# Performance work log

Hardware: AMD Instinct MI355X
Metric: run time of the kernel (lower is better)

## Reference

```python
import jax, jax.numpy as jnp
import numpy as np

N_NODES = 100000
N_EDGES = 1600000
D_FEAT = 256
HID = 128
DEG_DIM = 128  # data.degree_exist_matrix.shape[1]


def setup_inputs() -> dict:
    key = jax.random.key(0)
    ks = jax.random.split(key, 12)
    s = lambda fan_in: 1.0 / np.sqrt(fan_in)
    x = jax.random.normal(ks[0], (N_NODES, D_FEAT), dtype=jnp.float32)
    edge_index = jax.random.randint(ks[1], (2, N_EDGES), 0, N_NODES, dtype=jnp.int32)
    return {
        "x": x,
        "edge_index": edge_index,
        # GCNConv 1 / 2 (PyG stores weight [in,out], bias [out])
        "W1": jax.random.uniform(ks[2], (D_FEAT, HID), jnp.float32, -s(D_FEAT), s(D_FEAT)),
        "b1": jnp.zeros((HID,), jnp.float32),
        "W2": jax.random.uniform(ks[3], (HID, HID), jnp.float32, -s(HID), s(HID)),
        "b2": jnp.zeros((HID,), jnp.float32),
        # down_sample Linear(D_FEAT, HID)
        "Wd": jax.random.uniform(ks[4], (D_FEAT, HID), jnp.float32, -s(D_FEAT), s(D_FEAT)),
        "bd": jax.random.uniform(ks[5], (HID,), jnp.float32, -s(D_FEAT), s(D_FEAT)),
        # linear2: Degree_layer(HID, 1) ~ Linear(HID, 1)
        "Wdeg": jax.random.uniform(ks[6], (HID, 1), jnp.float32, -s(HID), s(HID)),
        "bdeg": jax.random.uniform(ks[7], (1,), jnp.float32, -s(HID), s(HID)),
        # linear3: Linear(HID, DEG_DIM)
        "W3": jax.random.uniform(ks[8], (HID, DEG_DIM), jnp.float32, -s(HID), s(HID)),
        "b3": jax.random.uniform(ks[9], (DEG_DIM,), jnp.float32, -s(HID), s(HID)),
    }


def gcn_conv(x, W, b, src, dst, n):
    """PyG GCNConv: D^-1/2 (A+I) D^-1/2 X W + b (symmetric norm, self-loops)."""
    h = x @ W  # [N, out]
    deg = jax.ops.segment_sum(jnp.ones_like(dst, dtype=h.dtype), dst, num_segments=n) + 1.0
    dinv = jax.lax.rsqrt(deg)  # deg >= 1 from self loop
    coef = dinv[src] * dinv[dst]  # [E]
    msgs = h[src] * coef[:, None]  # [E, out] -- dominant gather
    agg = jax.ops.segment_sum(msgs, dst, num_segments=n)
    agg = agg + h * (dinv * dinv)[:, None]  # self-loop contribution
    return agg + b


def reference(x, edge_index, W1, b1, W2, b2, Wd, bd, Wdeg, bdeg, W3, b3):
    n = x.shape[0]
    src, dst = edge_index[0], edge_index[1]
    original_x = x @ Wd + bd
    h = gcn_conv(x, W1, b1, src, dst, n)
    h = jax.nn.relu(h)  # dropout is identity in eval mode
    h = gcn_conv(h, W2, b2, src, dst, n)
    h = h + original_x  # residual
    result1 = jax.nn.log_softmax(h, axis=-1)        # [N, HID]
    result2 = (h @ Wdeg + bdeg).squeeze(-1)          # [N]
    result3 = h @ W3 + b3                            # [N, DEG_DIM]
    return (result1, result2, result3)
```

## Files before the change

kernel.cpp:

```cpp
#include <hip/hip_runtime.h>


typedef __attribute__((ext_vector_type(8))) short bf16x8;
typedef __attribute__((ext_vector_type(4))) float f32x4;

#define CDIV(a, b) (((a) + (b) - 1) / (b))

#define GLOBAL_AS __attribute__((address_space(1)))
#define LDS_AS __attribute__((address_space(3)))

__device__ __forceinline__ void gload16(const void* g, void* l) {
  __builtin_amdgcn_global_load_lds((const GLOBAL_AS unsigned int*)g,
                                   (LDS_AS unsigned int*)l, 16, 0, 0);
}

__device__ __forceinline__ float b2f(unsigned short u) {
  union { unsigned int i; float f; } x; x.i = ((unsigned int)u) << 16; return x.f;
}
__device__ __forceinline__ unsigned short f2b(float f) {
  union { float f; unsigned int i; } x; x.f = f;
  unsigned int r = x.i + 0x7fffu + ((x.i >> 16) & 1u);
  return (unsigned short)(r >> 16);
}
__device__ __forceinline__ void add2(float& a0, float& a1, unsigned int u) {
  union { unsigned int i; float f; } lo, hi;
  lo.i = u << 16; hi.i = u & 0xffff0000u;
  a0 += lo.f; a1 += hi.f;
}
__device__ __forceinline__ unsigned int pack2(float lo, float hi) {
  return __builtin_amdgcn_perm(__float_as_uint(hi) + 0x8000u,
                               __float_as_uint(lo) + 0x8000u, 0x07060302u);
}


__global__ void k_wtrans4(const float* __restrict__ W1, const float* __restrict__ Wd,
                          const float* __restrict__ W2, const float* __restrict__ W3,
                          unsigned short* __restrict__ W1t, unsigned short* __restrict__ Wdt,
                          unsigned short* __restrict__ W2t, unsigned short* __restrict__ W3t,
                          int* __restrict__ deg, int* __restrict__ bcnt, int n) {
  int idx = blockIdx.x * blockDim.x + threadIdx.x;
  if (idx >= 98304) {
    idx -= 98304;
    if (idx < n) deg[idx] = 0;
    else if (idx - n < 512) bcnt[idx - n] = 0;
    return;
  }
  const float* in; unsigned short* out; int K, N;
  if (idx < 32768)       { in = W1; out = W1t; K = 256; N = 128; }
  else if (idx < 65536)  { in = Wd; out = Wdt; K = 256; N = 128; idx -= 32768; }
  else if (idx < 81920)  { in = W2; out = W2t; K = 128; N = 128; idx -= 65536; }
  else                   { in = W3; out = W3t; K = 128; N = 128; idx -= 81920; }
  int k = idx / N, nn = idx - k * N;
  out[nn * K + k] = f2b(in[idx]);
}

__global__ void k_scan1(const int* __restrict__ deg, int* __restrict__ lscan,
                        int* __restrict__ partials, float* __restrict__ dinv, int n) {
  __shared__ int sd[256];
  int tid = threadIdx.x;
  int base = blockIdx.x * 2048 + tid * 8;
  int v[8]; int tsum = 0;
#pragma unroll
  for (int i = 0; i < 8; ++i) {
    int idx = base + i;
    int xv = (idx < n) ? deg[idx] : 0;
    v[i] = xv; tsum += xv;
    if (idx < n) dinv[idx] = 1.0f / sqrtf((float)xv + 1.0f);
  }
  sd[tid] = tsum;
  __syncthreads();
  for (int off = 1; off < 256; off <<= 1) {
    int t = (tid >= off) ? sd[tid - off] : 0;
    __syncthreads();
    sd[tid] += t;
    __syncthreads();
  }
  int run = sd[tid] - tsum;
#pragma unroll
  for (int i = 0; i < 8; ++i) {
    int idx = base + i;
    if (idx < n) lscan[idx] = run;
    run += v[i];
  }
  if (tid == 255) partials[blockIdx.x] = sd[255];
}

__global__ void k_scan3(const int* __restrict__ partials, int* row_start,
                        int* __restrict__ cursor, int n, int E) {
  int idx = blockIdx.x * blockDim.x + threadIdx.x;
  if (idx >= n) return;
  int g = idx >> 11;
  int pre = 0;
  for (int i = 0; i < g; ++i) pre += partials[i];
  int v = row_start[idx] + pre;
  row_start[idx] = v;
  cursor[idx] = v;
  if (idx == 0) row_start[n] = E;
}


#define BIN_CHUNK 4096
#define OVF_CAP 65536

__global__ __launch_bounds__(256) void k_binA(
    const int* __restrict__ ei, int E, int nbuck, int cap,
    int* __restrict__ deg, int2* __restrict__ pairs, int* __restrict__ bcnt,
    int2* __restrict__ ovf, int* __restrict__ ovf_cnt) {
  __shared__ int lcnt[256];
  __shared__ int lbase[256];
  int tid = threadIdx.x;
  for (int i = tid; i < nbuck; i += 256) lcnt[i] = 0;
  __syncthreads();
  int base_e = blockIdx.x * BIN_CHUNK;
  int src[16], dst[16], lofs[16];
#pragma unroll
  for (int i = 0; i < 16; ++i) {
    int e = base_e + i * 256 + tid;
    if (e < E) {
      int s = ei[e], d = ei[E + e];
      src[i] = s; dst[i] = d;
      atomicAdd(&deg[d], 1);
      lofs[i] = atomicAdd(&lcnt[d >> 9], 1);
    } else {
      dst[i] = -1;
    }
  }
  __syncthreads();
  for (int b = tid; b < nbuck; b += 256)
    lbase[b] = atomicAdd(&bcnt[b], lcnt[b]);
  __syncthreads();
#pragma unroll
  for (int i = 0; i < 16; ++i) {
    if (dst[i] < 0) continue;
    int b = dst[i] >> 9;
    int gpos = lbase[b] + lofs[i];
    if (gpos < cap) {
      pairs[(size_t)b * cap + gpos] = make_int2(src[i], dst[i]);
    } else {
      int op = atomicAdd(ovf_cnt, 1);
      if (op < OVF_CAP) ovf[op] = make_int2(src[i], dst[i]);
    }
  }
}

__global__ __launch_bounds__(256) void k_binB(
    const int2* __restrict__ pairs, const int* __restrict__ bcnt,
    int nbuck, int cap,
    const int2* __restrict__ ovf, const int* __restrict__ ovf_cnt,
    int* __restrict__ cursor, int* __restrict__ csr_src, int n) {
  int ov = *ovf_cnt;
  if ((int)blockIdx.x < nbuck) {
    int b = blockIdx.x;
    int cnt = bcnt[b]; if (cnt > cap) cnt = cap;
    const int2* p = pairs + (size_t)b * cap;
    if (ov == 0) {
      __shared__ int lcur[512];
      int nbase = b << 9;
      for (int i = threadIdx.x; i < 512; i += 256) {
        int node = nbase + i;
        lcur[i] = (node < n) ? cursor[node] : 0;
      }
      __syncthreads();
      for (int i = threadIdx.x; i < cnt; i += 256) {
        int2 e = p[i];
        int pos = atomicAdd(&lcur[e.y - nbase], 1);
        csr_src[pos] = e.x;
      }
    } else {
      for (int i = threadIdx.x; i < cnt; i += 256) {
        int2 e = p[i];
        int pos = atomicAdd(&cursor[e.y], 1);
        csr_src[pos] = e.x;
      }
    }
  } else {
    int total = ov; if (total > OVF_CAP) total = OVF_CAP;
    int start = (blockIdx.x - nbuck) * 256 + threadIdx.x;
    for (int i = start; i < total; i += 8 * 256) {
      int2 e = ovf[i];
      int pos = atomicAdd(&cursor[e.y], 1);
      csr_src[pos] = e.x;
    }
  }
}


__global__ __launch_bounds__(512) void k_gemm_x2(
    const float* __restrict__ X,
    const unsigned short* __restrict__ B1t,
    const unsigned short* __restrict__ B2t,
    const float* __restrict__ bias2,
    const float* __restrict__ dinvp,
    unsigned short* __restrict__ O1,
    unsigned short* __restrict__ O2,
    int n) {
  __shared__ char lds[65536];
  const int flat = threadIdx.x;
  const int wave = flat >> 6, lane = flat & 63;
  const int l15 = lane & 15, q = lane >> 4;
  const int wM = wave >> 1, wN = wave & 1;
  const int rowBase = blockIdx.x * 128;
  const int colBase = wN * 64;

  auto stage = [&](int kb, int buf) {
    char* ldsA = lds + buf * 32768;
    char* ldsB = ldsA + 16384;
    const char* Xb = (const char*)X;
#pragma unroll
    for (int j = 0; j < 2; ++j) {
      int i = j * 512 + flat;
      int row = i >> 3, pslot = i & 7;
      int lslot = pslot ^ (row & 7);
      int rowc = rowBase + row; if (rowc >= n) rowc = n - 1;
      gload16(Xb + (size_t)rowc * 1024 + (size_t)(kb * 128 + lslot * 16),
              ldsA + (j * 512 + wave * 64) * 16);
    }
#pragma unroll
    for (int j = 0; j < 2; ++j) {
      int i = j * 512 + flat;
      int col = i >> 3, pslot = i & 7;
      int lslot = pslot ^ (col & 7);
      const char* src = (lslot >= 4) ? (const char*)B2t : (const char*)B1t;
      gload16(src + (size_t)col * 512 + kb * 64 + (lslot & 3) * 16,
              ldsB + (j * 512 + wave * 64) * 16);
    }
  };

  f32x4 acc1[2][4], acc2[2][4];
#pragma unroll
  for (int i = 0; i < 2; ++i)
#pragma unroll
    for (int j = 0; j < 4; ++j) {
      acc1[i][j] = (f32x4){0.f, 0.f, 0.f, 0.f};
      acc2[i][j] = (f32x4){0.f, 0.f, 0.f, 0.f};
    }

  stage(0, 0);
  stage(1, 1);

#pragma unroll
  for (int kb = 0; kb < 8; ++kb) {
    int cur = kb & 1;
    if (kb < 7) asm volatile("s_waitcnt vmcnt(4)" ::: "memory");
    else        asm volatile("s_waitcnt vmcnt(0)" ::: "memory");
    __builtin_amdgcn_s_barrier();
    char* ldsA = lds + cur * 32768;
    char* ldsB = ldsA + 16384;
    bf16x8 a[2], b1v[4], b2v[4];
#pragma unroll
    for (int mt = 0; mt < 2; ++mt) {
      int row = wM * 32 + mt * 16 + l15;
      uint4 lo = *(const uint4*)(ldsA + row * 128 + (((2 * q) ^ (row & 7)) * 16));
      uint4 hi = *(const uint4*)(ldsA + row * 128 + (((2 * q + 1) ^ (row & 7)) * 16));
      union { bf16x8 v; unsigned int u[4]; } r;
      r.u[0] = __builtin_amdgcn_perm(lo.y + 0x8000u, lo.x + 0x8000u, 0x07060302u);
      r.u[1] = __builtin_amdgcn_perm(lo.w + 0x8000u, lo.z + 0x8000u, 0x07060302u);
      r.u[2] = __builtin_amdgcn_perm(hi.y + 0x8000u, hi.x + 0x8000u, 0x07060302u);
      r.u[3] = __builtin_amdgcn_perm(hi.w + 0x8000u, hi.z + 0x8000u, 0x07060302u);
      a[mt] = r.v;
    }
#pragma unroll
    for (int nt = 0; nt < 4; ++nt) {
      int col = colBase + nt * 16 + l15;
      b1v[nt] = *(const bf16x8*)(ldsB + col * 128 + ((q ^ (col & 7)) * 16));
      b2v[nt] = *(const bf16x8*)(ldsB + col * 128 + (((4 + q) ^ (col & 7)) * 16));
    }
#pragma unroll
    for (int mt = 0; mt < 2; ++mt)
#pragma unroll
      for (int nt = 0; nt < 4; ++nt) {
        acc1[mt][nt] = __builtin_amdgcn_mfma_f32_16x16x32_bf16(a[mt], b1v[nt], acc1[mt][nt], 0, 0, 0);
        acc2[mt][nt] = __builtin_amdgcn_mfma_f32_16x16x32_bf16(a[mt], b2v[nt], acc2[mt][nt], 0, 0, 0);
      }
    asm volatile("s_waitcnt lgkmcnt(0)" ::: "memory");
    __builtin_amdgcn_s_barrier();
    if (kb < 6) stage(kb + 2, cur);
  }

#pragma unroll
  for (int mt = 0; mt < 2; ++mt) {
    float4 dv = *(const float4*)(dinvp + rowBase + wM * 32 + mt * 16 + q * 4);
#pragma unroll
    for (int nt = 0; nt < 4; ++nt) {
      int col = colBase + nt * 16 + l15;
      float bb = bias2[col];
#pragma unroll
      for (int r = 0; r < 4; ++r) {
        int row = rowBase + wM * 32 + mt * 16 + q * 4 + r;
        if (row < n) {
          float dvr = (r == 0) ? dv.x : (r == 1) ? dv.y : (r == 2) ? dv.z : dv.w;
          O1[(size_t)row * 128 + col] = f2b(acc1[mt][nt][r] * dvr);
          O2[(size_t)row * 128 + col] = f2b(acc2[mt][nt][r] + bb);
        }
      }
    }
  }
}

template <int OUT_F32>
__global__ __launch_bounds__(512) void k_gemm_h(
    const unsigned short* __restrict__ X, const unsigned short* __restrict__ Bt,
    const float* __restrict__ bias, const float* __restrict__ dinvp,
    unsigned short* __restrict__ Ob, float* __restrict__ Of, int n) {
  __shared__ char lds[65536];
  const int flat = threadIdx.x;
  const int wave = flat >> 6, lane = flat & 63;
  const int l15 = lane & 15, q = lane >> 4;
  const int wM = wave >> 1, wN = wave & 1;
  const int rowBase = blockIdx.x * 128;
  const int colBase = wN * 64;

  auto stage = [&](int ks, int buf) {
    char* ldsA = lds + buf * 32768;
    char* ldsB = ldsA + 16384;
#pragma unroll
    for (int j = 0; j < 2; ++j) {
      int i = j * 512 + flat;
      int row = i >> 3, pslot = i & 7;
      int lslot = pslot ^ (row & 7);
      int rowc = rowBase + row; if (rowc >= n) rowc = n - 1;
      gload16((const char*)X + (size_t)rowc * 256 + ks * 128 + lslot * 16,
              ldsA + (j * 512 + wave * 64) * 16);
    }
#pragma unroll
    for (int j = 0; j < 2; ++j) {
      int i = j * 512 + flat;
      int col = i >> 3, pslot = i & 7;
      int lslot = pslot ^ (col & 7);
      gload16((const char*)Bt + (size_t)col * 256 + ks * 128 + lslot * 16,
              ldsB + (j * 512 + wave * 64) * 16);
    }
  };

  f32x4 acc[2][4];
#pragma unroll
  for (int i = 0; i < 2; ++i)
#pragma unroll
    for (int j = 0; j < 4; ++j) acc[i][j] = (f32x4){0.f, 0.f, 0.f, 0.f};

  stage(0, 0);
  stage(1, 1);

#pragma unroll
  for (int ks = 0; ks < 2; ++ks) {
    if (ks == 0) asm volatile("s_waitcnt vmcnt(4)" ::: "memory");
    else         asm volatile("s_waitcnt vmcnt(0)" ::: "memory");
    __builtin_amdgcn_s_barrier();
    char* ldsA = lds + ks * 32768;
    char* ldsB = ldsA + 16384;
#pragma unroll
    for (int k2 = 0; k2 < 2; ++k2) {
      bf16x8 a[2], b[4];
#pragma unroll
      for (int mt = 0; mt < 2; ++mt) {
        int row = wM * 32 + mt * 16 + l15;
        a[mt] = *(const bf16x8*)(ldsA + row * 128 + (((k2 * 4 + q) ^ (row & 7)) * 16));
      }
#pragma unroll
      for (int nt = 0; nt < 4; ++nt) {
        int col = colBase + nt * 16 + l15;
        b[nt] = *(const bf16x8*)(ldsB + col * 128 + (((k2 * 4 + q) ^ (col & 7)) * 16));
      }
#pragma unroll
      for (int mt = 0; mt < 2; ++mt)
#pragma unroll
        for (int nt = 0; nt < 4; ++nt)
          acc[mt][nt] = __builtin_amdgcn_mfma_f32_16x16x32_bf16(a[mt], b[nt], acc[mt][nt], 0, 0, 0);
    }
  }

#pragma unroll
  for (int mt = 0; mt < 2; ++mt) {
    float4 dv;
    if (!OUT_F32) dv = *(const float4*)(dinvp + rowBase + wM * 32 + mt * 16 + q * 4);
#pragma unroll
    for (int nt = 0; nt < 4; ++nt) {
      int col = colBase + nt * 16 + l15;
      float bb = OUT_F32 ? bias[col] : 0.f;
#pragma unroll
      for (int r = 0; r < 4; ++r) {
        int row = rowBase + wM * 32 + mt * 16 + q * 4 + r;
        if (row < n) {
          if (OUT_F32) {
            __builtin_nontemporal_store(acc[mt][nt][r] + bb, &Of[(size_t)row * 128 + col]);
          } else {
            float dvr = (r == 0) ? dv.x : (r == 1) ? dv.y : (r == 2) ? dv.z : dv.w;
            Ob[(size_t)row * 128 + col] = f2b(acc[mt][nt][r] * dvr);
          }
        }
      }
    }
  }
}


__device__ __forceinline__ void agg_edges4(
    const unsigned short* __restrict__ h, const int* __restrict__ csr_src,
    int beg, int end, int lane, int grp, int sub, float* acc) {
  for (int base = beg; base < end; base += 64) {
    int m = end - base; if (m > 64) m = 64;
    int idx_l = (base + lane < end) ? csr_src[base + lane] : 0;
    for (int j = 0; j < m; j += 16) {
      int s0 = __builtin_amdgcn_ds_bpermute((j + grp) << 2, idx_l);
      int s1 = __builtin_amdgcn_ds_bpermute((j + 4 + grp) << 2, idx_l);
      int s2 = __builtin_amdgcn_ds_bpermute((j + 8 + grp) << 2, idx_l);
      int s3 = __builtin_amdgcn_ds_bpermute((j + 12 + grp) << 2, idx_l);
      uint4 v0 = *(const uint4*)(h + (size_t)s0 * 128 + sub * 8);
      uint4 v1 = *(const uint4*)(h + (size_t)s1 * 128 + sub * 8);
      uint4 v2 = *(const uint4*)(h + (size_t)s2 * 128 + sub * 8);
      uint4 v3 = *(const uint4*)(h + (size_t)s3 * 128 + sub * 8);
      if (j + grp < m) {
        add2(acc[0], acc[1], v0.x); add2(acc[2], acc[3], v0.y);
        add2(acc[4], acc[5], v0.z); add2(acc[6], acc[7], v0.w);
      }
      if (j + 4 + grp < m) {
        add2(acc[0], acc[1], v1.x); add2(acc[2], acc[3], v1.y);
        add2(acc[4], acc[5], v1.z); add2(acc[6], acc[7], v1.w);
      }
      if (j + 8 + grp < m) {
        add2(acc[0], acc[1], v2.x); add2(acc[2], acc[3], v2.y);
        add2(acc[4], acc[5], v2.z); add2(acc[6], acc[7], v2.w);
      }
      if (j + 12 + grp < m) {
        add2(acc[0], acc[1], v3.x); add2(acc[2], acc[3], v3.y);
        add2(acc[4], acc[5], v3.z); add2(acc[6], acc[7], v3.w);
      }
    }
  }
}

__device__ __forceinline__ void grp_reduce(float* acc) {
#pragma unroll
  for (int i = 0; i < 8; ++i) {
    acc[i] += __shfl_xor(acc[i], 16);
    acc[i] += __shfl_xor(acc[i], 32);
  }
}

__global__ __launch_bounds__(256) void k_agg1(
    const unsigned short* __restrict__ h,
    const int* __restrict__ row_start, const int* __restrict__ csr_src,
    const float* __restrict__ dinv,
    const float* __restrict__ bias,
    unsigned short* __restrict__ hout, int n) {
  int gw = blockIdx.x * 4 + (threadIdx.x >> 6);
  int lane = threadIdx.x & 63;
  int grp = lane >> 4, sub = lane & 15;
  if (gw >= n) return;
  int beg = row_start[gw], end = row_start[gw + 1];
  float acc[8] = {0.f, 0.f, 0.f, 0.f, 0.f, 0.f, 0.f, 0.f};
  agg_edges4(h, csr_src, beg, end, lane, grp, sub, acc);
  grp_reduce(acc);
  if (grp == 0) {
    float dg = dinv[gw];
    uint4 sv = *(const uint4*)(h + (size_t)gw * 128 + sub * 8);
    add2(acc[0], acc[1], sv.x); add2(acc[2], acc[3], sv.y);
    add2(acc[4], acc[5], sv.z); add2(acc[6], acc[7], sv.w);
    float4 b0 = *(const float4*)(bias + sub * 8);
    float4 b1v = *(const float4*)(bias + sub * 8 + 4);
    float a[8];
    a[0] = fmaxf(acc[0] * dg + b0.x, 0.f); a[1] = fmaxf(acc[1] * dg + b0.y, 0.f);
    a[2] = fmaxf(acc[2] * dg + b0.z, 0.f); a[3] = fmaxf(acc[3] * dg + b0.w, 0.f);
    a[4] = fmaxf(acc[4] * dg + b1v.x, 0.f); a[5] = fmaxf(acc[5] * dg + b1v.y, 0.f);
    a[6] = fmaxf(acc[6] * dg + b1v.z, 0.f); a[7] = fmaxf(acc[7] * dg + b1v.w, 0.f);
    uint4 o;
    o.x = pack2(a[0], a[1]); o.y = pack2(a[2], a[3]);
    o.z = pack2(a[4], a[5]); o.w = pack2(a[6], a[7]);
    *(uint4*)(hout + (size_t)gw * 128 + sub * 8) = o;
  }
}

__global__ __launch_bounds__(256) void k_agg2_epi(
    const unsigned short* __restrict__ h,
    const int* __restrict__ row_start, const int* __restrict__ csr_src,
    const float* __restrict__ dinv,
    const float* __restrict__ bias,
    const unsigned short* __restrict__ resb,
    float* __restrict__ out1,
    const float* __restrict__ wdeg, const float* __restrict__ bdeg,
    float* __restrict__ out2,
    unsigned short* __restrict__ hf,
    int n) {
  int gw = blockIdx.x * 4 + (threadIdx.x >> 6);
  int lane = threadIdx.x & 63;
  int grp = lane >> 4, sub = lane & 15;
  if (gw >= n) return;
  int beg = row_start[gw], end = row_start[gw + 1];
  float acc[8] = {0.f, 0.f, 0.f, 0.f, 0.f, 0.f, 0.f, 0.f};
  agg_edges4(h, csr_src, beg, end, lane, grp, sub, acc);
  grp_reduce(acc);
  if (grp == 0) {
    float dg = dinv[gw];
    uint4 sv = *(const uint4*)(h + (size_t)gw * 128 + sub * 8);
    add2(acc[0], acc[1], sv.x); add2(acc[2], acc[3], sv.y);
    add2(acc[4], acc[5], sv.z); add2(acc[6], acc[7], sv.w);
    float4 b0 = *(const float4*)(bias + sub * 8);
    float4 b1v = *(const float4*)(bias + sub * 8 + 4);
    uint4 rv = *(const uint4*)(resb + (size_t)gw * 128 + sub * 8);
    float a[8];
    a[0] = acc[0] * dg + b0.x; a[1] = acc[1] * dg + b0.y;
    a[2] = acc[2] * dg + b0.z; a[3] = acc[3] * dg + b0.w;
    a[4] = acc[4] * dg + b1v.x; a[5] = acc[5] * dg + b1v.y;
    a[6] = acc[6] * dg + b1v.z; a[7] = acc[7] * dg + b1v.w;
    add2(a[0], a[1], rv.x); add2(a[2], a[3], rv.y);
    add2(a[4], a[5], rv.z); add2(a[6], a[7], rv.w);
    uint4 o;
    o.x = pack2(a[0], a[1]); o.y = pack2(a[2], a[3]);
    o.z = pack2(a[4], a[5]); o.w = pack2(a[6], a[7]);
    *(uint4*)(hf + (size_t)gw * 128 + sub * 8) = o;
    float4 w0 = *(const float4*)(wdeg + sub * 8);
    float4 w1 = *(const float4*)(wdeg + sub * 8 + 4);
    float t = a[0] * w0.x + a[1] * w0.y + a[2] * w0.z + a[3] * w0.w +
              a[4] * w1.x + a[5] * w1.y + a[6] * w1.z + a[7] * w1.w;
#pragma unroll
    for (int mk = 8; mk >= 1; mk >>= 1) t += __shfl_xor(t, mk);
    if (sub == 0) __builtin_nontemporal_store(t + bdeg[0], out2 + gw);
    float mx = a[0];
#pragma unroll
    for (int i = 1; i < 8; ++i) mx = fmaxf(mx, a[i]);
#pragma unroll
    for (int mk = 8; mk >= 1; mk >>= 1) mx = fmaxf(mx, __shfl_xor(mx, mk));
    float l = 0.f;
#pragma unroll
    for (int i = 0; i < 8; ++i) l += __expf(a[i] - mx);
#pragma unroll
    for (int mk = 8; mk >= 1; mk >>= 1) l += __shfl_xor(l, mk);
    float ls = mx + __logf(l);
    f32x4 o0 = {a[0] - ls, a[1] - ls, a[2] - ls, a[3] - ls};
    f32x4 o1 = {a[4] - ls, a[5] - ls, a[6] - ls, a[7] - ls};
    __builtin_nontemporal_store(o0, (f32x4*)(out1 + (size_t)gw * 128 + sub * 8));
    __builtin_nontemporal_store(o1, (f32x4*)(out1 + (size_t)gw * 128 + sub * 8 + 4));
  }
}


extern "C" void kernel_launch(void* const* d_in, const int* in_sizes, int n_in,
                              void* d_out, int out_size, void* d_ws, size_t ws_size,
                              hipStream_t stream) {
  const float* x   = (const float*)d_in[0];
  const int*   ei  = (const int*)d_in[1];
  const float* W1  = (const float*)d_in[2];
  const float* b1  = (const float*)d_in[3];
  const float* W2  = (const float*)d_in[4];
  const float* b2  = (const float*)d_in[5];
  const float* Wd  = (const float*)d_in[6];
  const float* bd  = (const float*)d_in[7];
  const float* Wdg = (const float*)d_in[8];
  const float* bdg = (const float*)d_in[9];
  const float* W3  = (const float*)d_in[10];
  const float* b3  = (const float*)d_in[11];

  const int N = in_sizes[0] / 256;
  const int E = in_sizes[1] / 2;

  char* w = (char*)d_ws;
  auto alloc = [&](size_t bytes) {
    char* p = w;
    w += (bytes + 255) & ~(size_t)255;
    return p;
  };
  unsigned short* W1t  = (unsigned short*)alloc((size_t)256 * 128 * 2);
  unsigned short* Wdt  = (unsigned short*)alloc((size_t)256 * 128 * 2);
  unsigned short* W2t  = (unsigned short*)alloc((size_t)128 * 128 * 2);
  unsigned short* W3t  = (unsigned short*)alloc((size_t)128 * 128 * 2);
  unsigned short* bufC = (unsigned short*)alloc((size_t)N * 128 * 2);
  int*   deg      = (int*)alloc((size_t)N * 4);
  float* dinv     = (float*)alloc((size_t)(N + 128) * 4);
  int*   row_start= (int*)alloc((size_t)(N + 1) * 4);
  int*   cursor   = (int*)alloc((size_t)N * 4);
  int*   partials = (int*)alloc(4096);
  int*   csr_src  = (int*)alloc((size_t)E * 4);
  int*   bcnt     = (int*)alloc(2048);
  int*   ovf_cnt  = bcnt + 256;
  int2*  ovf      = (int2*)alloc((size_t)OVF_CAP * 8);

  float* out1 = (float*)d_out;
  float* out2 = out1 + (size_t)N * 128;
  float* out3 = out2 + (size_t)N;
  unsigned short* bufA = (unsigned short*)out3;
  unsigned short* resb = bufA + (size_t)N * 128;

  const int nbuck = CDIV(N, 512);
  int cap = (E / nbuck) + (E / nbuck) / 2;
  cap = (cap + 255) & ~255;
  size_t bufC_bytes = (size_t)N * 128 * 2;
  if ((size_t)nbuck * cap * 8 > bufC_bytes)
    cap = (int)(bufC_bytes / ((size_t)nbuck * 8));
  int2* pairs = (int2*)bufC;

  k_wtrans4<<<CDIV(98304 + N + 512, 256), 256, 0, stream>>>(
      W1, Wd, W2, W3, W1t, Wdt, W2t, W3t, deg, bcnt, N);

  k_binA<<<CDIV(E, BIN_CHUNK), 256, 0, stream>>>(ei, E, nbuck, cap, deg, pairs,
                                                 bcnt, ovf, ovf_cnt);

  const int nb = CDIV(N, 2048);
  k_scan1<<<nb, 256, 0, stream>>>(deg, row_start, partials, dinv, N);
  k_scan3<<<CDIV(N, 256), 256, 0, stream>>>(partials, row_start, cursor, N, E);

  k_gemm_x2<<<CDIV(N, 128), 512, 0, stream>>>(x, W1t, Wdt, bd, dinv, bufA, resb, N);

  k_binB<<<nbuck + 8, 256, 0, stream>>>(pairs, bcnt, nbuck, cap, ovf, ovf_cnt,
                                        cursor, csr_src, N);

  k_agg1<<<CDIV(N, 4), 256, 0, stream>>>(bufA, row_start, csr_src, dinv, b1, bufC, N);

  k_gemm_h<0><<<CDIV(N, 128), 512, 0, stream>>>(bufC, W2t, nullptr, dinv, bufA, nullptr, N);

  k_agg2_epi<<<CDIV(N, 4), 256, 0, stream>>>(bufA, row_start, csr_src, dinv,
                                             b2, resb, out1, Wdg, bdg, out2, bufC, N);

  k_gemm_h<1><<<CDIV(N, 128), 512, 0, stream>>>(bufC, W3t, b3, nullptr, nullptr, out3, N);
}
```

Baseline: 497.3 us.

## Fuse degree count, scan and CSR scatter into one per-bucket kernel

```diff
diff --git a/kernel.cpp b/kernel.cpp
--- a/kernel.cpp
+++ b/kernel.cpp
@@ -37,12 +37,11 @@
                           const float* __restrict__ W2, const float* __restrict__ W3,
                           unsigned short* __restrict__ W1t, unsigned short* __restrict__ Wdt,
                           unsigned short* __restrict__ W2t, unsigned short* __restrict__ W3t,
-                          int* __restrict__ deg, int* __restrict__ bcnt, int n) {
+                          int* __restrict__ bcnt) {
   int idx = blockIdx.x * blockDim.x + threadIdx.x;
   if (idx >= 98304) {
     idx -= 98304;
-    if (idx < n) deg[idx] = 0;
-    else if (idx - n < 512) bcnt[idx - n] = 0;
+    if (idx < 512) bcnt[idx] = 0;
     return;
   }
   const float* in; unsigned short* out; int K, N;
@@ -54,57 +53,13 @@
   out[nn * K + k] = f2b(in[idx]);
 }
 
-__global__ void k_scan1(const int* __restrict__ deg, int* __restrict__ lscan,
-                        int* __restrict__ partials, float* __restrict__ dinv, int n) {
-  __shared__ int sd[256];
-  int tid = threadIdx.x;
-  int base = blockIdx.x * 2048 + tid * 8;
-  int v[8]; int tsum = 0;
-#pragma unroll
-  for (int i = 0; i < 8; ++i) {
-    int idx = base + i;
-    int xv = (idx < n) ? deg[idx] : 0;
-    v[i] = xv; tsum += xv;
-    if (idx < n) dinv[idx] = 1.0f / sqrtf((float)xv + 1.0f);
-  }
-  sd[tid] = tsum;
-  __syncthreads();
-  for (int off = 1; off < 256; off <<= 1) {
-    int t = (tid >= off) ? sd[tid - off] : 0;
-    __syncthreads();
-    sd[tid] += t;
-    __syncthreads();
-  }
-  int run = sd[tid] - tsum;
-#pragma unroll
-  for (int i = 0; i < 8; ++i) {
-    int idx = base + i;
-    if (idx < n) lscan[idx] = run;
-    run += v[i];
-  }
-  if (tid == 255) partials[blockIdx.x] = sd[255];
-}
-
-__global__ void k_scan3(const int* __restrict__ partials, int* row_start,
-                        int* __restrict__ cursor, int n, int E) {
-  int idx = blockIdx.x * blockDim.x + threadIdx.x;
-  if (idx >= n) return;
-  int g = idx >> 11;
-  int pre = 0;
-  for (int i = 0; i < g; ++i) pre += partials[i];
-  int v = row_start[idx] + pre;
-  row_start[idx] = v;
-  cursor[idx] = v;
-  if (idx == 0) row_start[n] = E;
-}
-
 
 #define BIN_CHUNK 4096
 #define OVF_CAP 65536
 
 __global__ __launch_bounds__(256) void k_binA(
     const int* __restrict__ ei, int E, int nbuck, int cap,
-    int* __restrict__ deg, int2* __restrict__ pairs, int* __restrict__ bcnt,
+    int2* __restrict__ pairs, int* __restrict__ bcnt,
     int2* __restrict__ ovf, int* __restrict__ ovf_cnt) {
   __shared__ int lcnt[256];
   __shared__ int lbase[256];
@@ -119,7 +74,6 @@
     if (e < E) {
       int s = ei[e], d = ei[E + e];
       src[i] = s; dst[i] = d;
-      atomicAdd(&deg[d], 1);
       lofs[i] = atomicAdd(&lcnt[d >> 9], 1);
     } else {
       dst[i] = -1;
@@ -143,43 +97,78 @@
   }
 }
 
-__global__ __launch_bounds__(256) void k_binB(
+__global__ __launch_bounds__(256) void k_binBC(
     const int2* __restrict__ pairs, const int* __restrict__ bcnt,
     int nbuck, int cap,
     const int2* __restrict__ ovf, const int* __restrict__ ovf_cnt,
-    int* __restrict__ cursor, int* __restrict__ csr_src, int n) {
-  int ov = *ovf_cnt;
-  if ((int)blockIdx.x < nbuck) {
-    int b = blockIdx.x;
-    int cnt = bcnt[b]; if (cnt > cap) cnt = cap;
-    const int2* p = pairs + (size_t)b * cap;
-    if (ov == 0) {
-      __shared__ int lcur[512];
-      int nbase = b << 9;
-      for (int i = threadIdx.x; i < 512; i += 256) {
-        int node = nbase + i;
-        lcur[i] = (node < n) ? cursor[node] : 0;
-      }
-      __syncthreads();
-      for (int i = threadIdx.x; i < cnt; i += 256) {
-        int2 e = p[i];
-        int pos = atomicAdd(&lcur[e.y - nbase], 1);
+    float* __restrict__ dinv, int* __restrict__ row_start,
+    int* __restrict__ csr_src, int n, int E) {
+  __shared__ int hist[512];
+  __shared__ int sb[256];
+  const int b = blockIdx.x;
+  const int tid = threadIdx.x;
+  const int nbase = b << 9;
+  hist[tid] = 0; hist[tid + 256] = 0;
+  __syncthreads();
+  int total = bcnt[b];
+  int cnt = (total < cap) ? total : cap;
+  const int2* p = pairs + (size_t)b * cap;
+  for (int i = tid; i < cnt; i += 256)
+    atomicAdd(&hist[p[i].y - nbase], 1);
+  int ov = *ovf_cnt; if (ov > OVF_CAP) ov = OVF_CAP;
+  if (ov > 0) {
+    for (int i = tid; i < ov; i += 256) {
+      int2 e = ovf[i];
+      if ((e.y >> 9) == b) atomicAdd(&hist[e.y - nbase], 1);
+    }
+  }
+  __syncthreads();
+  int h0 = hist[2 * tid], h1 = hist[2 * tid + 1];
+  sb[tid] = (tid < nbuck) ? bcnt[tid] : 0;
+  __syncthreads();
+  for (int off = 1; off < 256; off <<= 1) {
+    int t = (tid >= off) ? sb[tid - off] : 0;
+    __syncthreads();
+    sb[tid] += t;
+    __syncthreads();
+  }
+  int gbase = (b > 0) ? sb[b - 1] : 0;
+  __syncthreads();
+  sb[tid] = h0 + h1;
+  __syncthreads();
+  for (int off = 1; off < 256; off <<= 1) {
+    int t = (tid >= off) ? sb[tid - off] : 0;
+    __syncthreads();
+    sb[tid] += t;
+    __syncthreads();
+  }
+  int exc = (tid > 0) ? sb[tid - 1] : 0;
+  int c0 = gbase + exc, c1 = gbase + exc + h0;
+  int node0 = nbase + 2 * tid, node1 = node0 + 1;
+  if (node0 < n) {
+    dinv[node0] = 1.0f / sqrtf((float)h0 + 1.0f);
+    row_start[node0] = c0;
+  }
+  if (node1 < n) {
+    dinv[node1] = 1.0f / sqrtf((float)h1 + 1.0f);
+    row_start[node1] = c1;
+  }
+  if (b == 0 && tid == 0) row_start[n] = E;
+  __syncthreads();
+  hist[2 * tid] = c0; hist[2 * tid + 1] = c1;
+  __syncthreads();
+  for (int i = tid; i < cnt; i += 256) {
+    int2 e = p[i];
+    int pos = atomicAdd(&hist[e.y - nbase], 1);
+    csr_src[pos] = e.x;
+  }
+  if (ov > 0) {
+    for (int i = tid; i < ov; i += 256) {
+      int2 e = ovf[i];
+      if ((e.y >> 9) == b) {
+        int pos = atomicAdd(&hist[e.y - nbase], 1);
         csr_src[pos] = e.x;
       }
-    } else {
-      for (int i = threadIdx.x; i < cnt; i += 256) {
-        int2 e = p[i];
-        int pos = atomicAdd(&cursor[e.y], 1);
-        csr_src[pos] = e.x;
-      }
-    }
-  } else {
-    int total = ov; if (total > OVF_CAP) total = OVF_CAP;
-    int start = (blockIdx.x - nbuck) * 256 + threadIdx.x;
-    for (int i = start; i < total; i += 8 * 256) {
-      int2 e = ovf[i];
-      int pos = atomicAdd(&cursor[e.y], 1);
-      csr_src[pos] = e.x;
     }
   }
 }
@@ -564,11 +553,8 @@
   unsigned short* W2t  = (unsigned short*)alloc((size_t)128 * 128 * 2);
   unsigned short* W3t  = (unsigned short*)alloc((size_t)128 * 128 * 2);
   unsigned short* bufC = (unsigned short*)alloc((size_t)N * 128 * 2);
-  int*   deg      = (int*)alloc((size_t)N * 4);
   float* dinv     = (float*)alloc((size_t)(N + 128) * 4);
   int*   row_start= (int*)alloc((size_t)(N + 1) * 4);
-  int*   cursor   = (int*)alloc((size_t)N * 4);
-  int*   partials = (int*)alloc(4096);
   int*   csr_src  = (int*)alloc((size_t)E * 4);
   int*   bcnt     = (int*)alloc(2048);
   int*   ovf_cnt  = bcnt + 256;
@@ -588,20 +574,16 @@
     cap = (int)(bufC_bytes / ((size_t)nbuck * 8));
   int2* pairs = (int2*)bufC;
 
-  k_wtrans4<<<CDIV(98304 + N + 512, 256), 256, 0, stream>>>(
-      W1, Wd, W2, W3, W1t, Wdt, W2t, W3t, deg, bcnt, N);
-
-  k_binA<<<CDIV(E, BIN_CHUNK), 256, 0, stream>>>(ei, E, nbuck, cap, deg, pairs,
+  k_wtrans4<<<CDIV(98304 + 512, 256), 256, 0, stream>>>(
+      W1, Wd, W2, W3, W1t, Wdt, W2t, W3t, bcnt);
+
+  k_binA<<<CDIV(E, BIN_CHUNK), 256, 0, stream>>>(ei, E, nbuck, cap, pairs,
                                                  bcnt, ovf, ovf_cnt);
 
-  const int nb = CDIV(N, 2048);
-  k_scan1<<<nb, 256, 0, stream>>>(deg, row_start, partials, dinv, N);
-  k_scan3<<<CDIV(N, 256), 256, 0, stream>>>(partials, row_start, cursor, N, E);
+  k_binBC<<<nbuck, 256, 0, stream>>>(pairs, bcnt, nbuck, cap, ovf, ovf_cnt,
+                                     dinv, row_start, csr_src, N, E);
 
   k_gemm_x2<<<CDIV(N, 128), 512, 0, stream>>>(x, W1t, Wdt, bd, dinv, bufA, resb, N);
-
-  k_binB<<<nbuck + 8, 256, 0, stream>>>(pairs, bcnt, nbuck, cap, ovf, ovf_cnt,
-                                        cursor, csr_src, N);
 
   k_agg1<<<CDIV(N, 4), 256, 0, stream>>>(bufA, row_start, csr_src, dinv, b1, bufC, N);
 
```

New measurement: 441.6 us. -11.2%, faster.
